# Performance work log

Hardware: AMD Instinct MI355X
Metric: run time of the kernel (lower is better)

The kernel has to match this reference:

```python
import jax, jax.numpy as jnp
import numpy as np

SPATIAL = ((100, 100), (50, 50), (25, 25), (13, 13))
STARTS = [0]
for _h, _w in SPATIAL[:-1]:
    STARTS.append(STARTS[-1] + _h * _w)
L_TOTAL = sum(h * w for h, w in SPATIAL)  # 13294
D, DFFN, NL, NH, NP = 256, 1024, 4, 8, 4
DH = D // NH
EPS = 1e-5


def _ln(x, g, b):
    mu = x.mean(-1, keepdims=True)
    var = ((x - mu) ** 2).mean(-1, keepdims=True)
    return (x - mu) * jax.lax.rsqrt(var + EPS) * g + b


def _bilinear(v_l, x, y, H, W):
    # v_l: [B,NH,H*W,DH]; x,y: [B,NH,Q*NP] pixel coords (grid_sample align_corners=False, zero padding)
    x0f = jnp.floor(x); y0f = jnp.floor(y)
    lx, ly = x - x0f, y - y0f
    x0 = x0f.astype(jnp.int32); y0 = y0f.astype(jnp.int32)
    acc = 0.0
    for dx, dy, w in ((0, 0, (1 - lx) * (1 - ly)), (1, 0, lx * (1 - ly)),
                      (0, 1, (1 - lx) * ly), (1, 1, lx * ly)):
        xi, yi = x0 + dx, y0 + dy
        valid = (xi >= 0) & (xi < W) & (yi >= 0) & (yi < H)
        idx = jnp.clip(yi, 0, H - 1) * W + jnp.clip(xi, 0, W - 1)
        g = jnp.take_along_axis(v_l, idx[..., None], axis=2)  # [B,NH,Q*NP,DH]
        acc = acc + g * (w * valid.astype(w.dtype))[..., None]
    return acc


def _msdeform(query, value_in, ref, norm_wh, Woff, boff, Wattn, battn, Wval, bval, Wout, bout):
    B, Q, _ = query.shape
    v = (value_in @ Wval + bval).reshape(B, L_TOTAL, NH, DH)
    off = (query @ Woff + boff).reshape(B, Q, NH, NL, NP, 2)
    aw = (query @ Wattn + battn).reshape(B, Q, NH, NL * NP)
    aw = jax.nn.softmax(aw, axis=-1).reshape(B, Q, NH, NL, NP)
    # normalized sampling locations in [0,1]: ref + offset / (W,H)
    loc = ref[:, :, None, :, None, :] + off / norm_wh[None, None, None, :, None, :]
    out = 0.0
    for l, (H, W) in enumerate(SPATIAL):
        s = STARTS[l]
        v_l = v[:, s:s + H * W].transpose(0, 2, 1, 3)          # [B,NH,HW,DH]
        loc_l = loc[:, :, :, l].transpose(0, 2, 1, 3, 4)       # [B,NH,Q,NP,2]
        x = (loc_l[..., 0] * W - 0.5).reshape(B, NH, Q * NP)
        y = (loc_l[..., 1] * H - 0.5).reshape(B, NH, Q * NP)
        samp = _bilinear(v_l, x, y, H, W).reshape(B, NH, Q, NP, DH)
        w_l = aw[:, :, :, l].transpose(0, 2, 1, 3)             # [B,NH,Q,NP]
        out = out + (samp * w_l[..., None]).sum(3)             # [B,NH,Q,DH]
    out = out.transpose(0, 2, 1, 3).reshape(B, Q, D)
    return out @ Wout + bout


def setup_inputs() -> dict:
    key = jax.random.key(0)
    ks = jax.random.split(key, 12)
    B = 4
    s = 0.02
    return {
        "src": jax.random.normal(ks[0], (B, L_TOTAL, D), jnp.float32),
        "pos": jax.random.normal(ks[1], (B, L_TOTAL, D), jnp.float32),
        "reference_points": jax.random.uniform(ks[2], (B, L_TOTAL, NL, 2), jnp.float32),
        "spatial_shapes": jnp.array(SPATIAL, jnp.int32),
        "level_start_index": jnp.array(STARTS, jnp.int32),
        "W_off": jax.random.normal(ks[3], (D, NH * NL * NP * 2), jnp.float32) * 0.01,
        "b_off": jax.random.normal(ks[4], (NH * NL * NP * 2,), jnp.float32) * 0.5,
        "W_attn": jax.random.normal(ks[5], (D, NH * NL * NP), jnp.float32) * s,
        "b_attn": jnp.zeros((NH * NL * NP,), jnp.float32),
        "W_val": jax.random.normal(ks[6], (D, D), jnp.float32) * s,
        "b_val": jnp.zeros((D,), jnp.float32),
        "W_out": jax.random.normal(ks[7], (D, D), jnp.float32) * s,
        "b_out": jnp.zeros((D,), jnp.float32),
        "ln_sa_g": jnp.ones((D,), jnp.float32),
        "ln_sa_b": jnp.zeros((D,), jnp.float32),
        "W1": jax.random.normal(ks[8], (D, DFFN), jnp.float32) * s,
        "b1": jnp.zeros((DFFN,), jnp.float32),
        "W2": jax.random.normal(ks[9], (DFFN, D), jnp.float32) * s,
        "b2": jnp.zeros((D,), jnp.float32),
        "ln_ff_g": jnp.ones((D,), jnp.float32),
        "ln_ff_b": jnp.zeros((D,), jnp.float32),
    }


def reference(src, pos, reference_points, spatial_shapes, level_start_index,
              W_off, b_off, W_attn, b_attn, W_val, b_val, W_out, b_out,
              ln_sa_g, ln_sa_b, W1, b1, W2, b2, ln_ff_g, ln_ff_b):
    # offset normalizer is (W, H) per level
    norm_wh = jnp.stack([spatial_shapes[:, 1], spatial_shapes[:, 0]], -1).astype(src.dtype)
    q = src + pos  # with_pos_embed
    sa = _msdeform(q, src, reference_points, norm_wh,
                   W_off, b_off, W_attn, b_attn, W_val, b_val, W_out, b_out)
    x = _ln(sa + src, ln_sa_g, ln_sa_b)          # dropout = identity (eval)
    y = jnp.maximum(x @ W1 + b1, 0.0) @ W2 + b2  # relu FFN
    return _ln(y + x, ln_ff_g, ln_ff_b)
```

## Files before the change

### kernel.cpp

```cpp
#include <hip/hip_runtime.h>
#include <hip/hip_bf16.h>

typedef __hip_bfloat16 bf16;
typedef short bf16x8 __attribute__((ext_vector_type(8)));
typedef float f32x4  __attribute__((ext_vector_type(4)));

#define ROWS 53176
#define LTOT 13294

__device__ __forceinline__ float b2f(bf16 v) { return __bfloat162float(v); }

__device__ __forceinline__ void gl2lds16(const void* g, void* l) {
    __builtin_amdgcn_global_load_lds(
        (const __attribute__((address_space(1))) unsigned*)g,
        (__attribute__((address_space(3))) unsigned*)l, 16, 0, 0);
}

template<bool RELU>
__global__ __launch_bounds__(256)
void mfma_gemm_n(const bf16* __restrict__ A, const bf16* __restrict__ Bt,
                 const float* __restrict__ bias, bf16* __restrict__ C,
                 int M, int N, int K)
{
    __shared__ __align__(16) short As[128 * 32];
    __shared__ __align__(16) short Bs[128 * 32];
    const int tid  = threadIdx.x;
    const int wave = tid >> 6, lane = tid & 63;
    const int m0 = blockIdx.y * 128, n0 = blockIdx.x * 128;
    const int lrow = lane >> 2, lcol = lane & 3;
    const int quad = lane >> 4;

    f32x4 acc[4][4];
#pragma unroll
    for (int i = 0; i < 4; ++i)
#pragma unroll
        for (int j = 0; j < 4; ++j) acc[i][j] = (f32x4){0.f, 0.f, 0.f, 0.f};

    const int wM = (wave >> 1) * 64, wN = (wave & 1) * 64;
    const int foff = (lane & 15) * 32 + quad * 8;

    for (int kk = 0; kk < K; kk += 32) {
#pragma unroll
        for (int q = 0; q < 2; ++q) {
            int rbase = wave * 32 + q * 16;
            int row = rbase + lrow;
            gl2lds16(A  + (size_t)(m0 + row) * K + kk + lcol * 8, &As[rbase * 32]);
            gl2lds16(Bt + (size_t)(n0 + row) * K + kk + lcol * 8, &Bs[rbase * 32]);
        }
        __syncthreads();
        bf16x8 af[4], bfr[4];
#pragma unroll
        for (int i = 0; i < 4; ++i)
            af[i] = *(const bf16x8*)&As[(wM + i * 16) * 32 + foff];
#pragma unroll
        for (int j = 0; j < 4; ++j)
            bfr[j] = *(const bf16x8*)&Bs[(wN + j * 16) * 32 + foff];
#pragma unroll
        for (int i = 0; i < 4; ++i)
#pragma unroll
            for (int j = 0; j < 4; ++j)
                acc[i][j] = __builtin_amdgcn_mfma_f32_16x16x32_bf16(bfr[j], af[i], acc[i][j], 0, 0, 0);
        __syncthreads();
    }

    float4 b4[4];
#pragma unroll
    for (int j = 0; j < 4; ++j)
        b4[j] = *(const float4*)&bias[n0 + wN + j * 16 + quad * 4];

#pragma unroll
    for (int i = 0; i < 4; ++i) {
        int gm = m0 + wM + i * 16 + (lane & 15);
        if (gm >= M) continue;
#pragma unroll
        for (int j = 0; j < 4; ++j) {
            int gn = n0 + wN + j * 16 + quad * 4;
            union { bf16 h[4]; uint2 u2; } pk;
#pragma unroll
            for (int r = 0; r < 4; ++r) {
                float v = acc[i][j][r] + ((const float*)&b4[j])[r];
                if (RELU) v = fmaxf(v, 0.f);
                pk.h[r] = __float2bfloat16(v);
            }
            *(uint2*)&C[(size_t)gm * N + gn] = pk.u2;
        }
    }
}

template<bool RES_BF16, typename OT>
__global__ __launch_bounds__(512)
void mfma_gemm_ln(const bf16* __restrict__ A, const bf16* __restrict__ Bt,
                  const float* __restrict__ bias, const void* __restrict__ res,
                  OT* __restrict__ C, const float* __restrict__ gam,
                  const float* __restrict__ bet, int M, int K)
{
    __shared__ __align__(16) short As[128 * 32];
    __shared__ __align__(16) short Bs[256 * 32];
    __shared__ float rsum[128], rsq[128];
    const int tid  = threadIdx.x;
    const int wave = tid >> 6, lane = tid & 63;
    const int m0 = blockIdx.x * 128;
    const int lrow = lane >> 2, lcol = lane & 3;
    const int quad = lane >> 4;
    if (tid < 128) { rsum[tid] = 0.f; rsq[tid] = 0.f; }

    f32x4 acc[4][4];
#pragma unroll
    for (int i = 0; i < 4; ++i)
#pragma unroll
        for (int j = 0; j < 4; ++j) acc[i][j] = (f32x4){0.f, 0.f, 0.f, 0.f};

    const int wM = (wave >> 2) * 64, wN = (wave & 3) * 64;
    const int foff = (lane & 15) * 32 + quad * 8;

    for (int kk = 0; kk < K; kk += 32) {
#pragma unroll
        for (int q = 0; q < 3; ++q) {
            int r = wave * 48 + q * 16;
            if (r < 128) {
                gl2lds16(A + (size_t)(m0 + r + lrow) * K + kk + lcol * 8, &As[r * 32]);
            } else {
                int rr = r - 128;
                gl2lds16(Bt + (size_t)(rr + lrow) * K + kk + lcol * 8, &Bs[rr * 32]);
            }
        }
        __syncthreads();
        bf16x8 af[4], bfr[4];
#pragma unroll
        for (int i = 0; i < 4; ++i)
            af[i] = *(const bf16x8*)&As[(wM + i * 16) * 32 + foff];
#pragma unroll
        for (int j = 0; j < 4; ++j)
            bfr[j] = *(const bf16x8*)&Bs[(wN + j * 16) * 32 + foff];
#pragma unroll
        for (int i = 0; i < 4; ++i)
#pragma unroll
            for (int j = 0; j < 4; ++j)
                acc[i][j] = __builtin_amdgcn_mfma_f32_16x16x32_bf16(bfr[j], af[i], acc[i][j], 0, 0, 0);
        __syncthreads();
    }

    float4 b4[4], g4[4], be4[4];
#pragma unroll
    for (int j = 0; j < 4; ++j) {
        int gn = wN + j * 16 + quad * 4;
        b4[j]  = *(const float4*)&bias[gn];
        g4[j]  = *(const float4*)&gam[gn];
        be4[j] = *(const float4*)&bet[gn];
    }

    float lsum[4], lsq[4];
#pragma unroll
    for (int i = 0; i < 4; ++i) {
        int gm = m0 + wM + i * 16 + (lane & 15);
        lsum[i] = 0.f; lsq[i] = 0.f;
#pragma unroll
        for (int j = 0; j < 4; ++j) {
            int gn = wN + j * 16 + quad * 4;
            float r4[4] = {0.f, 0.f, 0.f, 0.f};
            if (gm < M) {
                if (RES_BF16) {
                    uint2 ru = *(const uint2*)&((const bf16*)res)[(size_t)gm * 256 + gn];
                    const bf16* rh = (const bf16*)&ru;
#pragma unroll
                    for (int r = 0; r < 4; ++r) r4[r] = b2f(rh[r]);
                } else {
                    float4 rf = *(const float4*)&((const float*)res)[(size_t)gm * 256 + gn];
#pragma unroll
                    for (int r = 0; r < 4; ++r) r4[r] = ((const float*)&rf)[r];
                }
            }
#pragma unroll
            for (int r = 0; r < 4; ++r) {
                float v = acc[i][j][r] + ((const float*)&b4[j])[r] + r4[r];
                acc[i][j][r] = v;
                lsum[i] += v;
                lsq[i]  += v * v;
            }
        }
#pragma unroll
        for (int mask = 16; mask <= 32; mask <<= 1) {
            lsum[i] += __shfl_xor(lsum[i], mask);
            lsq[i]  += __shfl_xor(lsq[i], mask);
        }
    }
    if (quad == 0) {
#pragma unroll
        for (int i = 0; i < 4; ++i) {
            atomicAdd(&rsum[wM + i * 16 + (lane & 15)], lsum[i]);
            atomicAdd(&rsq [wM + i * 16 + (lane & 15)], lsq[i]);
        }
    }
    __syncthreads();

#pragma unroll
    for (int i = 0; i < 4; ++i) {
        int lr = wM + i * 16 + (lane & 15);
        int gm = m0 + lr;
        if (gm >= M) continue;
        float mean = rsum[lr] * (1.f / 256.f);
        float var  = rsq[lr] * (1.f / 256.f) - mean * mean;
        float rstd = rsqrtf(fmaxf(var, 0.f) + 1e-5f);
#pragma unroll
        for (int j = 0; j < 4; ++j) {
            int gn = wN + j * 16 + quad * 4;
            if constexpr (sizeof(OT) == 2) {
                union { bf16 h[4]; uint2 u2; } pk;
#pragma unroll
                for (int r = 0; r < 4; ++r)
                    pk.h[r] = __float2bfloat16((acc[i][j][r] - mean) * rstd *
                              ((const float*)&g4[j])[r] + ((const float*)&be4[j])[r]);
                *(uint2*)&((bf16*)C)[(size_t)gm * 256 + gn] = pk.u2;
            } else {
                float4 o;
#pragma unroll
                for (int r = 0; r < 4; ++r)
                    ((float*)&o)[r] = (acc[i][j][r] - mean) * rstd *
                              ((const float*)&g4[j])[r] + ((const float*)&be4[j])[r];
                *(float4*)&((float*)C)[(size_t)gm * 256 + gn] = o;
            }
        }
    }
}

__global__ void cast_qs_kernel(const float* __restrict__ s, const float* __restrict__ p,
                               bf16* __restrict__ sb, bf16* __restrict__ qb, int n4)
{
    int i = blockIdx.x * 256 + threadIdx.x;
    if (i >= n4) return;
    float4 sv = ((const float4*)s)[i];
    float4 pv = ((const float4*)p)[i];
    union { bf16 h[4]; uint2 u; } a, b;
    a.h[0] = __float2bfloat16(sv.x); a.h[1] = __float2bfloat16(sv.y);
    a.h[2] = __float2bfloat16(sv.z); a.h[3] = __float2bfloat16(sv.w);
    b.h[0] = __float2bfloat16(sv.x + pv.x); b.h[1] = __float2bfloat16(sv.y + pv.y);
    b.h[2] = __float2bfloat16(sv.z + pv.z); b.h[3] = __float2bfloat16(sv.w + pv.w);
    ((uint2*)sb)[i] = a.u;
    ((uint2*)qb)[i] = b.u;
}

__global__ void wt_cast_kernel(const float* __restrict__ W, bf16* __restrict__ Wt, int K, int N)
{
    int e = blockIdx.x * 256 + threadIdx.x;
    if (e >= K * N) return;
    int n = e / K, k = e - n * K;
    Wt[e] = __float2bfloat16(W[(size_t)k * N + n]);
}

__global__ void wcat_cast_kernel(const float* __restrict__ Woff, const float* __restrict__ Wattn,
                                 const float* __restrict__ boff, const float* __restrict__ battn,
                                 bf16* __restrict__ Wt, float* __restrict__ bcat)
{
    int e = blockIdx.x * 256 + threadIdx.x;
    if (e < 384) bcat[e] = (e < 256) ? boff[e] : battn[e - 256];
    if (e >= 384 * 256) return;
    int n = e >> 8, k = e & 255;
    float w = (n < 256) ? Woff[(size_t)k * 256 + n] : Wattn[(size_t)k * 128 + (n - 256)];
    Wt[e] = __float2bfloat16(w);
}

__global__ __launch_bounds__(256)
void sample_kernel(const bf16* __restrict__ v, const bf16* __restrict__ ocat,
                   const float* __restrict__ ref, bf16* __restrict__ samp)
{
    __shared__ int4 tab[16][33];
    const int tid = threadIdx.x;
    const int grp = tid >> 4, lane = tid & 15;
    const int gidx = blockIdx.x * 16 + grp;
    const int h = gidx & 7, bq = gidx >> 3, b = bq / LTOT;

    {
        const int p = lane, l = p >> 2, pp = p & 3;
        const int W = (l == 0) ? 100 : (l == 1) ? 50 : (l == 2) ? 25 : 13;
        const int S = (l == 0) ? 0 : (l == 1) ? 10000 : (l == 2) ? 12500 : 13125;
        const float fW = (float)W;
        float rx = ref[(size_t)bq * 8 + l * 2 + 0];
        float ry = ref[(size_t)bq * 8 + l * 2 + 1];
        const bf16* ob = ocat + (size_t)bq * 384;
        float ox = b2f(ob[h * 32 + l * 8 + pp * 2 + 0]);
        float oy = b2f(ob[h * 32 + l * 8 + pp * 2 + 1]);
        float lg = b2f(ob[256 + h * 16 + p]);
        float m = lg;
#pragma unroll
        for (int mask = 1; mask <= 8; mask <<= 1) m = fmaxf(m, __shfl_xor(m, mask));
        float ev = __expf(lg - m);
        float s = ev;
#pragma unroll
        for (int mask = 1; mask <= 8; mask <<= 1) s += __shfl_xor(s, mask);
        float wgt = ev / s;

        float x = (rx + ox / fW) * fW - 0.5f;
        float y = (ry + oy / fW) * fW - 0.5f;
        float x0f = floorf(x), y0f = floorf(y);
        float lx = x - x0f, ly = y - y0f;
        int x0 = (int)x0f, y0 = (int)y0f;
        float tw[4] = {(1.f - lx) * (1.f - ly), lx * (1.f - ly),
                       (1.f - lx) * ly,         lx * ly};
        const int base = (b * LTOT + S) * 512 + h * 64;
        int  o[4]; float w[4];
#pragma unroll
        for (int t = 0; t < 4; ++t) {
            int xi = x0 + (t & 1), yi = y0 + (t >> 1);
            bool ok = (xi >= 0) & (xi < W) & (yi >= 0) & (yi < W);
            o[t] = ok ? base + (yi * W + xi) * 512 : 0;
            w[t] = ok ? wgt * tw[t] : 0.f;
        }
        tab[grp][p * 2 + 0] = make_int4(o[0], __float_as_int(w[0]), o[1], __float_as_int(w[1]));
        tab[grp][p * 2 + 1] = make_int4(o[2], __float_as_int(w[2]), o[3], __float_as_int(w[3]));
    }
    __syncthreads();

    const int lofs = lane * 4;
    const char* vc = (const char*)v;
    float a0 = 0.f, a1 = 0.f;
#pragma unroll 4
    for (int e2 = 0; e2 < 32; ++e2) {
        int4 q = tab[grp][e2];
        unsigned u0 = *(const unsigned*)(vc + (size_t)(unsigned)(q.x + lofs));
        unsigned u1 = *(const unsigned*)(vc + (size_t)(unsigned)(q.z + lofs));
        float w0 = __int_as_float(q.y), w1 = __int_as_float(q.w);
        a0 += w0 * __uint_as_float(u0 << 16);
        a1 += w0 * __uint_as_float(u0 & 0xffff0000u);
        a0 += w1 * __uint_as_float(u1 << 16);
        a1 += w1 * __uint_as_float(u1 & 0xffff0000u);
    }
    union { struct { bf16 a, b; } h2; unsigned u; } r;
    r.h2.a = __float2bfloat16(a0);
    r.h2.b = __float2bfloat16(a1);
    *(unsigned*)((char*)samp + (size_t)gidx * 64 + lane * 4) = r.u;
}

extern "C" void kernel_launch(void* const* d_in, const int* in_sizes, int n_in,
                              void* d_out, int out_size, void* d_ws, size_t ws_size,
                              hipStream_t stream)
{
    const float* src     = (const float*)d_in[0];
    const float* pos     = (const float*)d_in[1];
    const float* ref     = (const float*)d_in[2];
    const float* W_off   = (const float*)d_in[5];
    const float* b_off   = (const float*)d_in[6];
    const float* W_attn  = (const float*)d_in[7];
    const float* b_attn  = (const float*)d_in[8];
    const float* W_val   = (const float*)d_in[9];
    const float* b_val   = (const float*)d_in[10];
    const float* W_out   = (const float*)d_in[11];
    const float* b_out   = (const float*)d_in[12];
    const float* ln_sa_g = (const float*)d_in[13];
    const float* ln_sa_b = (const float*)d_in[14];
    const float* W1      = (const float*)d_in[15];
    const float* b1      = (const float*)d_in[16];
    const float* W2      = (const float*)d_in[17];
    const float* b2      = (const float*)d_in[18];
    const float* ln_ff_g = (const float*)d_in[19];
    const float* ln_ff_b = (const float*)d_in[20];

    char* ws = (char*)d_ws;
    bf16* sb     = (bf16*)(ws);
    bf16* samp   = (bf16*)(ws);
    bf16* qb     = (bf16*)(ws + 27226112);
    bf16* vbuf   = (bf16*)(ws + 54452224);
    bf16* ocat   = (bf16*)(ws + 81678336);
    bf16* xb16   = (bf16*)(ws + 122517504);
    bf16* hbuf   = (bf16*)(ws);
    bf16* Wval_t = (bf16*)(ws + 149743616);
    bf16* Wcat_t = (bf16*)(ws + 149874688);
    float* bcat  = (float*)(ws + 150071296);
    bf16* Wout_t = (bf16*)(ws + 150072832);
    bf16* W1_t   = (bf16*)(ws + 150203904);
    bf16* W2_t   = (bf16*)(ws + 150728192);
    float* outf  = (float*)d_out;

    dim3 blk(256);

    cast_qs_kernel<<<dim3((ROWS * 64 + 255) / 256), blk, 0, stream>>>(src, pos, sb, qb, ROWS * 64);
    wt_cast_kernel<<<dim3((256 * 256 + 255) / 256),  blk, 0, stream>>>(W_val, Wval_t, 256, 256);
    wcat_cast_kernel<<<dim3((384 * 256 + 255) / 256), blk, 0, stream>>>(W_off, W_attn, b_off, b_attn, Wcat_t, bcat);
    wt_cast_kernel<<<dim3((256 * 256 + 255) / 256),  blk, 0, stream>>>(W_out, Wout_t, 256, 256);
    wt_cast_kernel<<<dim3((256 * 1024 + 255) / 256), blk, 0, stream>>>(W1, W1_t, 256, 1024);
    wt_cast_kernel<<<dim3((1024 * 256 + 255) / 256), blk, 0, stream>>>(W2, W2_t, 1024, 256);

    mfma_gemm_n<false><<<dim3(2, 416), blk, 0, stream>>>(sb, Wval_t, b_val, vbuf, ROWS, 256, 256);
    mfma_gemm_n<false><<<dim3(3, 416), blk, 0, stream>>>(qb, Wcat_t, bcat, ocat, ROWS, 384, 256);
    sample_kernel<<<dim3(ROWS * 8 / 16), blk, 0, stream>>>(vbuf, ocat, ref, samp);
    mfma_gemm_ln<false, bf16><<<dim3(416), dim3(512), 0, stream>>>(
        samp, Wout_t, b_out, src, xb16, ln_sa_g, ln_sa_b, ROWS, 256);
    mfma_gemm_n<true><<<dim3(8, 416), blk, 0, stream>>>(xb16, W1_t, b1, hbuf, ROWS, 1024, 256);
    mfma_gemm_ln<true, float><<<dim3(416), dim3(512), 0, stream>>>(
        hbuf, W2_t, b2, xb16, outf, ln_ff_g, ln_ff_b, ROWS, 1024);
}
```

Baseline: 510.1 us.

## Widen sampler loads, merge weight casts, read bf16 residual in first LN

The deformable sampling kernel now gives each thread four channels instead of two. It uses 8-byte value loads and packed float2 accumulation, with 32 head-groups per block and each lane building two table entries. The five weight transpose/cast launches are merged into one kernel to cut launch overhead. The first GEMM+LayerNorm now reads the residual from the bf16 copy of src instead of fp32, which halves that read but adds rounding error to the residual. To make that possible, samp moves into the qb region so the bf16 src stays intact.

```diff
diff --git a/kernel.cpp b/kernel.cpp
--- a/kernel.cpp
+++ b/kernel.cpp
@@ -4,6 +4,7 @@
 typedef __hip_bfloat16 bf16;
 typedef short bf16x8 __attribute__((ext_vector_type(8)));
 typedef float f32x4  __attribute__((ext_vector_type(4)));
+typedef float f32x2  __attribute__((ext_vector_type(2)));
 
 #define ROWS 53176
 #define LTOT 13294
@@ -87,10 +88,10 @@
     }
 }
 
-template<bool RES_BF16, typename OT>
+template<typename OT>
 __global__ __launch_bounds__(512)
 void mfma_gemm_ln(const bf16* __restrict__ A, const bf16* __restrict__ Bt,
-                  const float* __restrict__ bias, const void* __restrict__ res,
+                  const float* __restrict__ bias, const bf16* __restrict__ res,
                   OT* __restrict__ C, const float* __restrict__ gam,
                   const float* __restrict__ bet, int M, int K)
 {
@@ -159,16 +160,10 @@
             int gn = wN + j * 16 + quad * 4;
             float r4[4] = {0.f, 0.f, 0.f, 0.f};
             if (gm < M) {
-                if (RES_BF16) {
-                    uint2 ru = *(const uint2*)&((const bf16*)res)[(size_t)gm * 256 + gn];
-                    const bf16* rh = (const bf16*)&ru;
-#pragma unroll
-                    for (int r = 0; r < 4; ++r) r4[r] = b2f(rh[r]);
-                } else {
-                    float4 rf = *(const float4*)&((const float*)res)[(size_t)gm * 256 + gn];
-#pragma unroll
-                    for (int r = 0; r < 4; ++r) r4[r] = ((const float*)&rf)[r];
-                }
+                uint2 ru = *(const uint2*)&res[(size_t)gm * 256 + gn];
+                const bf16* rh = (const bf16*)&ru;
+#pragma unroll
+                for (int r = 0; r < 4; ++r) r4[r] = b2f(rh[r]);
             }
 #pragma unroll
             for (int r = 0; r < 4; ++r) {
@@ -239,95 +234,113 @@
     ((uint2*)qb)[i] = b.u;
 }
 
-__global__ void wt_cast_kernel(const float* __restrict__ W, bf16* __restrict__ Wt, int K, int N)
-{
-    int e = blockIdx.x * 256 + threadIdx.x;
-    if (e >= K * N) return;
-    int n = e / K, k = e - n * K;
-    Wt[e] = __float2bfloat16(W[(size_t)k * N + n]);
-}
-
-__global__ void wcat_cast_kernel(const float* __restrict__ Woff, const float* __restrict__ Wattn,
-                                 const float* __restrict__ boff, const float* __restrict__ battn,
-                                 bf16* __restrict__ Wt, float* __restrict__ bcat)
+__global__ void wcast_all(const float* __restrict__ Wval, const float* __restrict__ Woff,
+                          const float* __restrict__ Wattn, const float* __restrict__ Wout,
+                          const float* __restrict__ W1, const float* __restrict__ W2,
+                          const float* __restrict__ boff, const float* __restrict__ battn,
+                          bf16* __restrict__ Wval_t, bf16* __restrict__ Wcat_t,
+                          bf16* __restrict__ Wout_t, bf16* __restrict__ W1_t,
+                          bf16* __restrict__ W2_t, float* __restrict__ bcat)
 {
     int e = blockIdx.x * 256 + threadIdx.x;
     if (e < 384) bcat[e] = (e < 256) ? boff[e] : battn[e - 256];
-    if (e >= 384 * 256) return;
-    int n = e >> 8, k = e & 255;
-    float w = (n < 256) ? Woff[(size_t)k * 256 + n] : Wattn[(size_t)k * 128 + (n - 256)];
-    Wt[e] = __float2bfloat16(w);
+    if (e < 65536) {
+        int n = e >> 8, k = e & 255;
+        Wval_t[e] = __float2bfloat16(Wval[k * 256 + n]);
+    } else if (e < 163840) {
+        int i = e - 65536; int n = i >> 8, k = i & 255;
+        float w = (n < 256) ? Woff[k * 256 + n] : Wattn[k * 128 + (n - 256)];
+        Wcat_t[i] = __float2bfloat16(w);
+    } else if (e < 229376) {
+        int i = e - 163840; int n = i >> 8, k = i & 255;
+        Wout_t[i] = __float2bfloat16(Wout[k * 256 + n]);
+    } else if (e < 491520) {
+        int i = e - 229376; int n = i >> 8, k = i & 255;
+        W1_t[i] = __float2bfloat16(W1[k * 1024 + n]);
+    } else if (e < 753664) {
+        int i = e - 491520; int n = i >> 10, k = i & 1023;
+        W2_t[i] = __float2bfloat16(W2[k * 256 + n]);
+    }
 }
 
 __global__ __launch_bounds__(256)
 void sample_kernel(const bf16* __restrict__ v, const bf16* __restrict__ ocat,
                    const float* __restrict__ ref, bf16* __restrict__ samp)
 {
-    __shared__ int4 tab[16][33];
+    __shared__ int4 tab[32][33];
     const int tid = threadIdx.x;
-    const int grp = tid >> 4, lane = tid & 15;
-    const int gidx = blockIdx.x * 16 + grp;
+    const int grp = tid >> 3, lane = tid & 7;
+    const int gidx = blockIdx.x * 32 + grp;
     const int h = gidx & 7, bq = gidx >> 3, b = bq / LTOT;
 
     {
-        const int p = lane, l = p >> 2, pp = p & 3;
-        const int W = (l == 0) ? 100 : (l == 1) ? 50 : (l == 2) ? 25 : 13;
-        const int S = (l == 0) ? 0 : (l == 1) ? 10000 : (l == 2) ? 12500 : 13125;
-        const float fW = (float)W;
-        float rx = ref[(size_t)bq * 8 + l * 2 + 0];
-        float ry = ref[(size_t)bq * 8 + l * 2 + 1];
         const bf16* ob = ocat + (size_t)bq * 384;
-        float ox = b2f(ob[h * 32 + l * 8 + pp * 2 + 0]);
-        float oy = b2f(ob[h * 32 + l * 8 + pp * 2 + 1]);
-        float lg = b2f(ob[256 + h * 16 + p]);
-        float m = lg;
-#pragma unroll
-        for (int mask = 1; mask <= 8; mask <<= 1) m = fmaxf(m, __shfl_xor(m, mask));
-        float ev = __expf(lg - m);
-        float s = ev;
-#pragma unroll
-        for (int mask = 1; mask <= 8; mask <<= 1) s += __shfl_xor(s, mask);
-        float wgt = ev / s;
-
-        float x = (rx + ox / fW) * fW - 0.5f;
-        float y = (ry + oy / fW) * fW - 0.5f;
-        float x0f = floorf(x), y0f = floorf(y);
-        float lx = x - x0f, ly = y - y0f;
-        int x0 = (int)x0f, y0 = (int)y0f;
-        float tw[4] = {(1.f - lx) * (1.f - ly), lx * (1.f - ly),
-                       (1.f - lx) * ly,         lx * ly};
-        const int base = (b * LTOT + S) * 512 + h * 64;
-        int  o[4]; float w[4];
-#pragma unroll
-        for (int t = 0; t < 4; ++t) {
-            int xi = x0 + (t & 1), yi = y0 + (t >> 1);
-            bool ok = (xi >= 0) & (xi < W) & (yi >= 0) & (yi < W);
-            o[t] = ok ? base + (yi * W + xi) * 512 : 0;
-            w[t] = ok ? wgt * tw[t] : 0.f;
-        }
-        tab[grp][p * 2 + 0] = make_int4(o[0], __float_as_int(w[0]), o[1], __float_as_int(w[1]));
-        tab[grp][p * 2 + 1] = make_int4(o[2], __float_as_int(w[2]), o[3], __float_as_int(w[3]));
+        float lg0 = b2f(ob[256 + h * 16 + lane]);
+        float lg1 = b2f(ob[256 + h * 16 + lane + 8]);
+        float m = fmaxf(lg0, lg1);
+#pragma unroll
+        for (int mask = 1; mask <= 4; mask <<= 1) m = fmaxf(m, __shfl_xor(m, mask));
+        float e0 = __expf(lg0 - m), e1 = __expf(lg1 - m);
+        float s = e0 + e1;
+#pragma unroll
+        for (int mask = 1; mask <= 4; mask <<= 1) s += __shfl_xor(s, mask);
+        float inv = 1.f / s;
+        float pw[2] = {e0 * inv, e1 * inv};
+#pragma unroll
+        for (int pi = 0; pi < 2; ++pi) {
+            const int p = lane + pi * 8, l = p >> 2, pp = p & 3;
+            const int W = (l == 0) ? 100 : (l == 1) ? 50 : (l == 2) ? 25 : 13;
+            const int S = (l == 0) ? 0 : (l == 1) ? 10000 : (l == 2) ? 12500 : 13125;
+            const float fW = (float)W;
+            float rx = ref[(size_t)bq * 8 + l * 2 + 0];
+            float ry = ref[(size_t)bq * 8 + l * 2 + 1];
+            float ox = b2f(ob[h * 32 + l * 8 + pp * 2 + 0]);
+            float oy = b2f(ob[h * 32 + l * 8 + pp * 2 + 1]);
+            float x = (rx + ox / fW) * fW - 0.5f;
+            float y = (ry + oy / fW) * fW - 0.5f;
+            float x0f = floorf(x), y0f = floorf(y);
+            float lx = x - x0f, ly = y - y0f;
+            int x0 = (int)x0f, y0 = (int)y0f;
+            float tw[4] = {(1.f - lx) * (1.f - ly), lx * (1.f - ly),
+                           (1.f - lx) * ly,         lx * ly};
+            const int base = (b * LTOT + S) * 512 + h * 64;
+            int  o[4]; float w[4];
+#pragma unroll
+            for (int t = 0; t < 4; ++t) {
+                int xi = x0 + (t & 1), yi = y0 + (t >> 1);
+                bool ok = (xi >= 0) & (xi < W) & (yi >= 0) & (yi < W);
+                o[t] = ok ? base + (yi * W + xi) * 512 : 0;
+                w[t] = ok ? pw[pi] * tw[t] : 0.f;
+            }
+            tab[grp][p * 2 + 0] = make_int4(o[0], __float_as_int(w[0]), o[1], __float_as_int(w[1]));
+            tab[grp][p * 2 + 1] = make_int4(o[2], __float_as_int(w[2]), o[3], __float_as_int(w[3]));
+        }
     }
     __syncthreads();
 
-    const int lofs = lane * 4;
+    const int lofs = lane * 8;
     const char* vc = (const char*)v;
-    float a0 = 0.f, a1 = 0.f;
+    f32x2 a01 = (f32x2){0.f, 0.f}, a23 = (f32x2){0.f, 0.f};
 #pragma unroll 4
     for (int e2 = 0; e2 < 32; ++e2) {
         int4 q = tab[grp][e2];
-        unsigned u0 = *(const unsigned*)(vc + (size_t)(unsigned)(q.x + lofs));
-        unsigned u1 = *(const unsigned*)(vc + (size_t)(unsigned)(q.z + lofs));
+        uint2 u0 = *(const uint2*)(vc + (size_t)(unsigned)(q.x + lofs));
+        uint2 u1 = *(const uint2*)(vc + (size_t)(unsigned)(q.z + lofs));
         float w0 = __int_as_float(q.y), w1 = __int_as_float(q.w);
-        a0 += w0 * __uint_as_float(u0 << 16);
-        a1 += w0 * __uint_as_float(u0 & 0xffff0000u);
-        a0 += w1 * __uint_as_float(u1 << 16);
-        a1 += w1 * __uint_as_float(u1 & 0xffff0000u);
-    }
-    union { struct { bf16 a, b; } h2; unsigned u; } r;
-    r.h2.a = __float2bfloat16(a0);
-    r.h2.b = __float2bfloat16(a1);
-    *(unsigned*)((char*)samp + (size_t)gidx * 64 + lane * 4) = r.u;
+        f32x2 w0v = (f32x2){w0, w0}, w1v = (f32x2){w1, w1};
+        f32x2 c0 = (f32x2){__uint_as_float(u0.x << 16), __uint_as_float(u0.x & 0xffff0000u)};
+        f32x2 c1 = (f32x2){__uint_as_float(u0.y << 16), __uint_as_float(u0.y & 0xffff0000u)};
+        f32x2 c2 = (f32x2){__uint_as_float(u1.x << 16), __uint_as_float(u1.x & 0xffff0000u)};
+        f32x2 c3 = (f32x2){__uint_as_float(u1.y << 16), __uint_as_float(u1.y & 0xffff0000u)};
+        a01 += w0v * c0;  a23 += w0v * c1;
+        a01 += w1v * c2;  a23 += w1v * c3;
+    }
+    union { bf16 hh[4]; uint2 u; } r;
+    r.hh[0] = __float2bfloat16(a01.x);
+    r.hh[1] = __float2bfloat16(a01.y);
+    r.hh[2] = __float2bfloat16(a23.x);
+    r.hh[3] = __float2bfloat16(a23.y);
+    *(uint2*)((char*)samp + (size_t)gidx * 64 + lane * 8) = r.u;
 }
 
 extern "C" void kernel_launch(void* const* d_in, const int* in_sizes, int n_in,
@@ -356,8 +369,8 @@
 
     char* ws = (char*)d_ws;
     bf16* sb     = (bf16*)(ws);
-    bf16* samp   = (bf16*)(ws);
     bf16* qb     = (bf16*)(ws + 27226112);
+    bf16* samp   = (bf16*)(ws + 27226112);
     bf16* vbuf   = (bf16*)(ws + 54452224);
     bf16* ocat   = (bf16*)(ws + 81678336);
     bf16* xb16   = (bf16*)(ws + 122517504);
@@ -373,18 +386,16 @@
     dim3 blk(256);
 
     cast_qs_kernel<<<dim3((ROWS * 64 + 255) / 256), blk, 0, stream>>>(src, pos, sb, qb, ROWS * 64);
-    wt_cast_kernel<<<dim3((256 * 256 + 255) / 256),  blk, 0, stream>>>(W_val, Wval_t, 256, 256);
-    wcat_cast_kernel<<<dim3((384 * 256 + 255) / 256), blk, 0, stream>>>(W_off, W_attn, b_off, b_attn, Wcat_t, bcat);
-    wt_cast_kernel<<<dim3((256 * 256 + 255) / 256),  blk, 0, stream>>>(W_out, Wout_t, 256, 256);
-    wt_cast_kernel<<<dim3((256 * 1024 + 255) / 256), blk, 0, stream>>>(W1, W1_t, 256, 1024);
-    wt_cast_kernel<<<dim3((1024 * 256 + 255) / 256), blk, 0, stream>>>(W2, W2_t, 1024, 256);
+    wcast_all<<<dim3(2944), blk, 0, stream>>>(W_val, W_off, W_attn, W_out, W1, W2,
+                                              b_off, b_attn,
+                                              Wval_t, Wcat_t, Wout_t, W1_t, W2_t, bcat);
 
     mfma_gemm_n<false><<<dim3(2, 416), blk, 0, stream>>>(sb, Wval_t, b_val, vbuf, ROWS, 256, 256);
     mfma_gemm_n<false><<<dim3(3, 416), blk, 0, stream>>>(qb, Wcat_t, bcat, ocat, ROWS, 384, 256);
-    sample_kernel<<<dim3(ROWS * 8 / 16), blk, 0, stream>>>(vbuf, ocat, ref, samp);
-    mfma_gemm_ln<false, bf16><<<dim3(416), dim3(512), 0, stream>>>(
-        samp, Wout_t, b_out, src, xb16, ln_sa_g, ln_sa_b, ROWS, 256);
+    sample_kernel<<<dim3(ROWS * 8 / 32), blk, 0, stream>>>(vbuf, ocat, ref, samp);
+    mfma_gemm_ln<bf16><<<dim3(416), dim3(512), 0, stream>>>(
+        samp, Wout_t, b_out, sb, xb16, ln_sa_g, ln_sa_b, ROWS, 256);
     mfma_gemm_n<true><<<dim3(8, 416), blk, 0, stream>>>(xb16, W1_t, b1, hbuf, ROWS, 1024, 256);
-    mfma_gemm_ln<true, float><<<dim3(416), dim3(512), 0, stream>>>(
+    mfma_gemm_ln<float><<<dim3(416), dim3(512), 0, stream>>>(
         hbuf, W2_t, b2, xb16, outf, ln_ff_g, ln_ff_b, ROWS, 1024);
 }
```

New measurement: 528.7 us. 1.04x slower.
